# Performance work log

Measured on AMD Instinct MI355X. Metric: run time of the kernel, lower is better.

The kernel has to match this reference:

```python
import jax, jax.numpy as jnp
import numpy as np

B, S, N, D, M = 4, 4096, 16, 64, 4  # batch, seq, heads, head_dim, num_scales

def setup_inputs() -> dict:
    key = jax.random.key(0)
    ks = jax.random.split(key, 6)
    return {
        "q": jax.random.normal(ks[0], (B, S, N, D), dtype=jnp.float32),
        "k": jax.random.normal(ks[1], (B, S, N, D), dtype=jnp.float32),
        "v": jax.random.normal(ks[2], (B, S, N, D), dtype=jnp.float32),
        "memory": jax.random.normal(ks[3], (B, M, N, D, D), dtype=jnp.float32),
        "decay_factors": jax.random.uniform(ks[4], (M,), dtype=jnp.float32) + 0.5,
        "gate_weights": jax.random.uniform(ks[5], (M,), dtype=jnp.float32),
    }

def reference(q, k, v, memory, decay_factors, gate_weights):
    # --- update_memory: decayed outer-product accumulation ---
    # new_info[b,n,k,v] = sum_s k[b,s,n,k] * v[b,s,n,v]  (fused; never build [b,s,n,k,v])
    new_info = jnp.einsum('bsnk,bsnv->bnkv', k, v)
    sig = jax.nn.sigmoid(decay_factors)            # [M]
    sig5 = sig[None, :, None, None, None]          # [1,M,1,1,1]
    mem_new = memory * sig5 + (1.0 - sig5) * new_info[:, None]  # [B,M,N,D,D]
    # --- forward read: q @ memory per scale, softmax-gated scale mixing ---
    gates = jax.nn.softmax(gate_weights)           # [M]
    # fuse gate mixing into the contraction; never build [b,m,s,n,v]
    out = jnp.einsum('bsnk,bmnkv,m->bsnv', q, mem_new, gates)
    return out
```

## Files before the change

### kernel.cpp

```cpp
#include <hip/hip_runtime.h>
#include <hip/hip_bf16.h>
#include <math.h>

constexpr int B = 4, S = 4096, N = 16, D = 64, M = 4;
constexpr int SND = S * N * D;
constexpr int ND  = N * D;
constexpr int DD  = D * D;

typedef __attribute__((ext_vector_type(8))) short bf16x8;
typedef __attribute__((ext_vector_type(4))) float f32x4;
typedef unsigned short ushort_t;
typedef unsigned int uint_t;

__device__ inline ushort_t f2bf(float x) {
  __hip_bfloat16 h = __float2bfloat16(x);
  return __builtin_bit_cast(ushort_t, h);
}

__global__ __launch_bounds__(256) void k1_partials(const float* __restrict__ kg,
                                                   const float* __restrict__ vg,
                                                   float* __restrict__ part,
                                                   int spb) {
  __shared__ ushort_t kT[2][64][64];
  __shared__ ushort_t vT[2][64][64];

  const int t = threadIdx.x, w = t >> 6, l = t & 63;
  const int bn = blockIdx.x;
  const int b = bn >> 4, n = bn & 15;
  const size_t base = (size_t)b * SND + (size_t)n * D +
                      (size_t)blockIdx.y * spb * ND;

  const int ss2 = 16 * w + 2 * (l >> 3);
  const int d8  = (l & 7) * 8;
  const int m0  = (w >> 1) * 32, n0w = (w & 1) * 32;
  const int lr  = l & 15, lg = l >> 4;

  f32x4 acc[2][2];
#pragma unroll
  for (int i = 0; i < 2; ++i)
#pragma unroll
    for (int j = 0; j < 2; ++j) acc[i][j] = (f32x4)0.f;

  float ka[8], kb2[8], va[8], vb2[8];

#define K1_LOAD(st)                                                         \
  {                                                                         \
    const float* kp = kg + base + (size_t)((st) * 64 + ss2) * ND + d8;      \
    const float* vp = vg + base + (size_t)((st) * 64 + ss2) * ND + d8;      \
    *(float4*)&ka[0]  = *(const float4*)kp;                                 \
    *(float4*)&ka[4]  = *(const float4*)(kp + 4);                           \
    *(float4*)&kb2[0] = *(const float4*)(kp + ND);                          \
    *(float4*)&kb2[4] = *(const float4*)(kp + ND + 4);                      \
    *(float4*)&va[0]  = *(const float4*)vp;                                 \
    *(float4*)&va[4]  = *(const float4*)(vp + 4);                           \
    *(float4*)&vb2[0] = *(const float4*)(vp + ND);                          \
    *(float4*)&vb2[4] = *(const float4*)(vp + ND + 4);                      \
  }

#define K1_WRITE(buf)                                                       \
  {                                                                         \
    const int sl = ss2 >> 3, sw = ss2 & 7;                                  \
    _Pragma("unroll")                                                       \
    for (int i = 0; i < 8; ++i) {                                           \
      const int off = (((sl) ^ i) << 3) + sw;               \
      *(uint_t*)&kT[buf][d8 + i][off] =                                     \
          (uint_t)f2bf(ka[i]) | ((uint_t)f2bf(kb2[i]) << 16);               \
      *(uint_t*)&vT[buf][d8 + i][off] =                                     \
          (uint_t)f2bf(va[i]) | ((uint_t)f2bf(vb2[i]) << 16);               \
    }                                                                       \
  }

  K1_LOAD(0);
  K1_WRITE(0);

  const int nst = spb >> 6;
  for (int st = 0; st < nst; ++st) {
    if (st + 1 < nst) K1_LOAD(st + 1);
    __syncthreads();
    const int buf = st & 1;
#pragma unroll
    for (int ks = 0; ks < 2; ++ks) {
      const int sp = ((4 * ks + lg) ^ (lr & 7)) << 3;
      bf16x8 a0 = *(const bf16x8*)&kT[buf][m0 + lr][sp];
      bf16x8 a1 = *(const bf16x8*)&kT[buf][m0 + 16 + lr][sp];
      bf16x8 b0 = *(const bf16x8*)&vT[buf][n0w + lr][sp];
      bf16x8 b1 = *(const bf16x8*)&vT[buf][n0w + 16 + lr][sp];
      acc[0][0] = __builtin_amdgcn_mfma_f32_16x16x32_bf16(a0, b0, acc[0][0], 0, 0, 0);
      acc[0][1] = __builtin_amdgcn_mfma_f32_16x16x32_bf16(a0, b1, acc[0][1], 0, 0, 0);
      acc[1][0] = __builtin_amdgcn_mfma_f32_16x16x32_bf16(a1, b0, acc[1][0], 0, 0, 0);
      acc[1][1] = __builtin_amdgcn_mfma_f32_16x16x32_bf16(a1, b1, acc[1][1], 0, 0, 0);
    }
    if (st + 1 < nst) K1_WRITE((st + 1) & 1);
  }

  float* p = part + ((size_t)bn * gridDim.y + blockIdx.y) * DD;
#pragma unroll
  for (int mi = 0; mi < 2; ++mi)
#pragma unroll
    for (int ni = 0; ni < 2; ++ni)
#pragma unroll
      for (int ri = 0; ri < 4; ++ri)
        p[(m0 + 16 * mi + 4 * lg + ri) * 64 + (n0w + 16 * ni + lr)] =
            acc[mi][ni][ri];
#undef K1_LOAD
#undef K1_WRITE
}

__global__ __launch_bounds__(256) void k2_combine(const float* __restrict__ part,
                                                  const float* __restrict__ memg,
                                                  const float* __restrict__ decay,
                                                  const float* __restrict__ gatew,
                                                  ushort_t* __restrict__ meffT,
                                                  int nchunks) {
  const int t = threadIdx.x;
  const int bn = blockIdx.x;
  const int b = bn >> 4, n = bn & 15;
  const int kv = blockIdx.y * 256 + t;
  const int k = kv >> 6, v = kv & 63;

  float gw[M], df[M];
#pragma unroll
  for (int m = 0; m < M; ++m) { gw[m] = gatew[m]; df[m] = decay[m]; }
  const float mx = fmaxf(fmaxf(gw[0], gw[1]), fmaxf(gw[2], gw[3]));
  float e[M], esum = 0.f;
#pragma unroll
  for (int m = 0; m < M; ++m) { e[m] = expf(gw[m] - mx); esum += e[m]; }
  float wgt[M], c = 0.f;
#pragma unroll
  for (int m = 0; m < M; ++m) {
    const float g = e[m] / esum;
    const float sg = 1.f / (1.f + expf(-df[m]));
    wgt[m] = g * sg;
    c += g * (1.f - sg);
  }

  const float* pb = part + (size_t)bn * nchunks * DD + kv;
  float ni = 0.f;
  for (int ch = 0; ch < nchunks; ++ch) ni += pb[(size_t)ch * DD];
  float a = c * ni;
#pragma unroll
  for (int m = 0; m < M; ++m)
    a += wgt[m] * memg[(((size_t)b * M + m) * N + n) * DD + kv];

  meffT[(size_t)bn * DD + v * 64 + k] = f2bf(a);
}

__global__ __launch_bounds__(256, 4) void k3_out(const float* __restrict__ qg,
                                                 const ushort_t* __restrict__ meffT,
                                                 float* __restrict__ outg) {
  const int t = threadIdx.x, w = t >> 6, l = t & 63;
  const int lr = l & 15, lg = l >> 4;
  const int bn = blockIdx.x;
  const int b = bn >> 4, n = bn & 15;
  const int s0 = blockIdx.y * 256 + w * 64;

  const ushort_t* mb = meffT + (size_t)bn * DD;
  bf16x8 bfr[4][2];
#pragma unroll
  for (int ni = 0; ni < 4; ++ni)
#pragma unroll
    for (int ks = 0; ks < 2; ++ks)
      bfr[ni][ks] = *(const bf16x8*)(mb + (16 * ni + lr) * 64 + 32 * ks + 8 * lg);

  f32x4 acc[4][4];
#pragma unroll
  for (int i = 0; i < 4; ++i)
#pragma unroll
    for (int j = 0; j < 4; ++j) acc[i][j] = (f32x4)0.f;

  const size_t qbase = (size_t)b * SND + (size_t)n * D;

#pragma unroll
  for (int mi = 0; mi < 4; ++mi) {
    const float* qr = qg + qbase + (size_t)(s0 + 16 * mi + lr) * ND + 8 * lg;
#pragma unroll
    for (int ks = 0; ks < 2; ++ks) {
      float qa[8];
      *(float4*)&qa[0] = *(const float4*)(qr + 32 * ks);
      *(float4*)&qa[4] = *(const float4*)(qr + 32 * ks + 4);
      bf16x8 a;
#pragma unroll
      for (int j = 0; j < 8; ++j) a[j] = (short)f2bf(qa[j]);
#pragma unroll
      for (int ni = 0; ni < 4; ++ni)
        acc[mi][ni] = __builtin_amdgcn_mfma_f32_16x16x32_bf16(a, bfr[ni][ks],
                                                              acc[mi][ni], 0, 0, 0);
    }
  }

#pragma unroll
  for (int mi = 0; mi < 4; ++mi)
#pragma unroll
    for (int ni = 0; ni < 4; ++ni)
#pragma unroll
      for (int ri = 0; ri < 4; ++ri)
        outg[qbase + (size_t)(s0 + 16 * mi + 4 * lg + ri) * ND + 16 * ni + lr] =
            acc[mi][ni][ri];
}

extern "C" void kernel_launch(void* const* d_in, const int* in_sizes, int n_in,
                              void* d_out, int out_size, void* d_ws, size_t ws_size,
                              hipStream_t stream) {
  const float* q     = (const float*)d_in[0];
  const float* k     = (const float*)d_in[1];
  const float* v     = (const float*)d_in[2];
  const float* memg  = (const float*)d_in[3];
  const float* decay = (const float*)d_in[4];
  const float* gatew = (const float*)d_in[5];
  float* out = (float*)d_out;

  ushort_t* meffT = (ushort_t*)d_ws;
  const size_t meffT_bytes = (size_t)64 * DD * sizeof(ushort_t);
  float* part = (float*)((char*)d_ws + meffT_bytes);

  const size_t avail = ws_size > meffT_bytes ? ws_size - meffT_bytes : 0;
  int nchunks = 16;
  while (nchunks > 1 && (size_t)nchunks * 64 * DD * sizeof(float) > avail)
    nchunks >>= 1;
  const int spb = S / nchunks;

  hipLaunchKernelGGL(k1_partials, dim3(64, nchunks), dim3(256), 0, stream,
                     k, v, part, spb);
  hipLaunchKernelGGL(k2_combine, dim3(64, 16), dim3(256), 0, stream,
                     part, memg, decay, gatew, meffT, nchunks);
  hipLaunchKernelGGL(k3_out, dim3(64, 16), dim3(256), 0, stream,
                     q, meffT, out);
}
```

Before: 71.27 us.

## Give each wave its own sequence slice in k1 and reduce partials in LDS

The k/v outer-product kernel now gives each of the four waves a private 128-row sequence slice and a full 64x64 accumulator tile. Each wave double-buffers its own LDS region, so the per-stage block-wide __syncthreads is gone, and the four wave partials are summed through LDS before a single store. The chunk count is fixed at 8 instead of 16, which halves the k1 grid and the partial traffic read by k2. In exchange k1 launches fewer blocks, so parallelism drops, each thread holds more accumulator registers, and the workspace-size fallback is removed.

```diff
diff --git a/kernel.cpp b/kernel.cpp
--- a/kernel.cpp
+++ b/kernel.cpp
@@ -6,112 +6,132 @@
 constexpr int SND = S * N * D;
 constexpr int ND  = N * D;
 constexpr int DD  = D * D;
+constexpr int NCH = 8;
+constexpr int SPB = S / NCH;
 
 typedef __attribute__((ext_vector_type(8))) short bf16x8;
 typedef __attribute__((ext_vector_type(4))) float f32x4;
-typedef unsigned short ushort_t;
-typedef unsigned int uint_t;
-
-__device__ inline ushort_t f2bf(float x) {
+typedef unsigned short u16;
+typedef unsigned int u32;
+
+__device__ inline u16 f2bf(float x) {
   __hip_bfloat16 h = __float2bfloat16(x);
-  return __builtin_bit_cast(ushort_t, h);
+  return __builtin_bit_cast(u16, h);
 }
 
 __global__ __launch_bounds__(256) void k1_partials(const float* __restrict__ kg,
                                                    const float* __restrict__ vg,
-                                                   float* __restrict__ part,
-                                                   int spb) {
-  __shared__ ushort_t kT[2][64][64];
-  __shared__ ushort_t vT[2][64][64];
+                                                   float* __restrict__ part) {
+  __shared__ u16 lds[4][2][2][64][32];
 
   const int t = threadIdx.x, w = t >> 6, l = t & 63;
   const int bn = blockIdx.x;
   const int b = bn >> 4, n = bn & 15;
+  const int r = l & 7, c = l >> 3;
+  const int lr = l & 15, lg = l >> 4;
+
   const size_t base = (size_t)b * SND + (size_t)n * D +
-                      (size_t)blockIdx.y * spb * ND;
-
-  const int ss2 = 16 * w + 2 * (l >> 3);
-  const int d8  = (l & 7) * 8;
-  const int m0  = (w >> 1) * 32, n0w = (w & 1) * 32;
-  const int lr  = l & 15, lg = l >> 4;
-
-  f32x4 acc[2][2];
-#pragma unroll
-  for (int i = 0; i < 2; ++i)
-#pragma unroll
-    for (int j = 0; j < 2; ++j) acc[i][j] = (f32x4)0.f;
-
-  float ka[8], kb2[8], va[8], vb2[8];
-
-#define K1_LOAD(st)                                                         \
-  {                                                                         \
-    const float* kp = kg + base + (size_t)((st) * 64 + ss2) * ND + d8;      \
-    const float* vp = vg + base + (size_t)((st) * 64 + ss2) * ND + d8;      \
-    *(float4*)&ka[0]  = *(const float4*)kp;                                 \
-    *(float4*)&ka[4]  = *(const float4*)(kp + 4);                           \
-    *(float4*)&kb2[0] = *(const float4*)(kp + ND);                          \
-    *(float4*)&kb2[4] = *(const float4*)(kp + ND + 4);                      \
-    *(float4*)&va[0]  = *(const float4*)vp;                                 \
-    *(float4*)&va[4]  = *(const float4*)(vp + 4);                           \
-    *(float4*)&vb2[0] = *(const float4*)(vp + ND);                          \
-    *(float4*)&vb2[4] = *(const float4*)(vp + ND + 4);                      \
-  }
-
-#define K1_WRITE(buf)                                                       \
-  {                                                                         \
-    const int sl = ss2 >> 3, sw = ss2 & 7;                                  \
-    _Pragma("unroll")                                                       \
-    for (int i = 0; i < 8; ++i) {                                           \
-      const int off = (((sl) ^ i) << 3) + sw;               \
-      *(uint_t*)&kT[buf][d8 + i][off] =                                     \
-          (uint_t)f2bf(ka[i]) | ((uint_t)f2bf(kb2[i]) << 16);               \
-      *(uint_t*)&vT[buf][d8 + i][off] =                                     \
-          (uint_t)f2bf(va[i]) | ((uint_t)f2bf(vb2[i]) << 16);               \
-    }                                                                       \
-  }
-
-  K1_LOAD(0);
-  K1_WRITE(0);
-
-  const int nst = spb >> 6;
-  for (int st = 0; st < nst; ++st) {
-    if (st + 1 < nst) K1_LOAD(st + 1);
-    __syncthreads();
-    const int buf = st & 1;
-#pragma unroll
-    for (int ks = 0; ks < 2; ++ks) {
-      const int sp = ((4 * ks + lg) ^ (lr & 7)) << 3;
-      bf16x8 a0 = *(const bf16x8*)&kT[buf][m0 + lr][sp];
-      bf16x8 a1 = *(const bf16x8*)&kT[buf][m0 + 16 + lr][sp];
-      bf16x8 b0 = *(const bf16x8*)&vT[buf][n0w + lr][sp];
-      bf16x8 b1 = *(const bf16x8*)&vT[buf][n0w + 16 + lr][sp];
-      acc[0][0] = __builtin_amdgcn_mfma_f32_16x16x32_bf16(a0, b0, acc[0][0], 0, 0, 0);
-      acc[0][1] = __builtin_amdgcn_mfma_f32_16x16x32_bf16(a0, b1, acc[0][1], 0, 0, 0);
-      acc[1][0] = __builtin_amdgcn_mfma_f32_16x16x32_bf16(a1, b0, acc[1][0], 0, 0, 0);
-      acc[1][1] = __builtin_amdgcn_mfma_f32_16x16x32_bf16(a1, b1, acc[1][1], 0, 0, 0);
-    }
-    if (st + 1 < nst) K1_WRITE((st + 1) & 1);
-  }
-
-  float* p = part + ((size_t)bn * gridDim.y + blockIdx.y) * DD;
-#pragma unroll
-  for (int mi = 0; mi < 2; ++mi)
-#pragma unroll
-    for (int ni = 0; ni < 2; ++ni)
+                      ((size_t)blockIdx.y * SPB + (size_t)w * 128) * ND;
+
+  f32x4 acc[4][4];
+#pragma unroll
+  for (int i = 0; i < 4; ++i)
+#pragma unroll
+    for (int j = 0; j < 4; ++j) acc[i][j] = (f32x4)0.f;
+
+  float kfa[2][2][8], vfa[2][2][8];
+
+#define STAGE_LOAD(tt)                                                        \
+  {                                                                           \
+    _Pragma("unroll") for (int h = 0; h < 2; ++h)                             \
+    _Pragma("unroll") for (int sp = 0; sp < 2; ++sp) {                        \
+      const float* kp =                                                       \
+          kg + base + (size_t)((tt) * 32 + 16 * h + 2 * r + sp) * ND + 8 * c; \
+      const float* vp =                                                       \
+          vg + base + (size_t)((tt) * 32 + 16 * h + 2 * r + sp) * ND + 8 * c; \
+      *(float4*)&kfa[h][sp][0] = *(const float4*)kp;                          \
+      *(float4*)&kfa[h][sp][4] = *(const float4*)(kp + 4);                    \
+      *(float4*)&vfa[h][sp][0] = *(const float4*)vp;                          \
+      *(float4*)&vfa[h][sp][4] = *(const float4*)(vp + 4);                    \
+    }                                                                         \
+  }
+
+#define STAGE_WRITE(buf)                                                      \
+  {                                                                           \
+    _Pragma("unroll") for (int h = 0; h < 2; ++h)                             \
+    _Pragma("unroll") for (int dd = 0; dd < 8; ++dd) {                        \
+      const int d = 8 * c + dd;                                               \
+      const int slot = (((2 * h + (r >> 2)) ^ (d & 3)) << 3) + ((2 * r) & 7); \
+      *(u32*)&lds[w][buf][0][d][slot] =                                       \
+          (u32)f2bf(kfa[h][0][dd]) | ((u32)f2bf(kfa[h][1][dd]) << 16);        \
+      *(u32*)&lds[w][buf][1][d][slot] =                                       \
+          (u32)f2bf(vfa[h][0][dd]) | ((u32)f2bf(vfa[h][1][dd]) << 16);        \
+    }                                                                         \
+  }
+
+#define COMPUTE(buf)                                                          \
+  {                                                                           \
+    bf16x8 af[4], bfq[4];                                                     \
+    _Pragma("unroll") for (int mi = 0; mi < 4; ++mi) {                        \
+      const int row = 16 * mi + lr;                                           \
+      af[mi]  = *(const bf16x8*)&lds[w][buf][0][row][(lg ^ (row & 3)) << 3];  \
+      bfq[mi] = *(const bf16x8*)&lds[w][buf][1][row][(lg ^ (row & 3)) << 3];  \
+    }                                                                         \
+    _Pragma("unroll") for (int mi = 0; mi < 4; ++mi)                          \
+    _Pragma("unroll") for (int ni = 0; ni < 4; ++ni)                          \
+      acc[mi][ni] = __builtin_amdgcn_mfma_f32_16x16x32_bf16(                  \
+          af[mi], bfq[ni], acc[mi][ni], 0, 0, 0);                             \
+  }
+
+  STAGE_LOAD(0);
+  STAGE_WRITE(0);
+  STAGE_LOAD(1);
+  COMPUTE(0);
+  STAGE_WRITE(1);
+  STAGE_LOAD(2);
+  COMPUTE(1);
+  STAGE_WRITE(0);
+  STAGE_LOAD(3);
+  COMPUTE(0);
+  STAGE_WRITE(1);
+  COMPUTE(1);
+
+#undef STAGE_LOAD
+#undef STAGE_WRITE
+#undef COMPUTE
+
+  __syncthreads();
+  float* red = (float*)lds;
+#pragma unroll
+  for (int mi = 0; mi < 4; ++mi)
+#pragma unroll
+    for (int ni = 0; ni < 4; ++ni)
 #pragma unroll
       for (int ri = 0; ri < 4; ++ri)
-        p[(m0 + 16 * mi + 4 * lg + ri) * 64 + (n0w + 16 * ni + lr)] =
+        red[w * 4096 + (16 * mi + 4 * lg + ri) * 64 + 16 * ni + lr] =
             acc[mi][ni][ri];
-#undef K1_LOAD
-#undef K1_WRITE
+  __syncthreads();
+
+  float* p = part + ((size_t)bn * NCH + blockIdx.y) * DD;
+#pragma unroll
+  for (int j = 0; j < 4; ++j) {
+    const int e = t * 16 + 4 * j;
+    const float4 a0 = *(const float4*)&red[e];
+    const float4 a1 = *(const float4*)&red[4096 + e];
+    const float4 a2 = *(const float4*)&red[8192 + e];
+    const float4 a3 = *(const float4*)&red[12288 + e];
+    *(float4*)&p[e] = make_float4(a0.x + a1.x + a2.x + a3.x,
+                                  a0.y + a1.y + a2.y + a3.y,
+                                  a0.z + a1.z + a2.z + a3.z,
+                                  a0.w + a1.w + a2.w + a3.w);
+  }
 }
 
 __global__ __launch_bounds__(256) void k2_combine(const float* __restrict__ part,
                                                   const float* __restrict__ memg,
                                                   const float* __restrict__ decay,
                                                   const float* __restrict__ gatew,
-                                                  ushort_t* __restrict__ meffT,
-                                                  int nchunks) {
+                                                  u16* __restrict__ meffT) {
   const int t = threadIdx.x;
   const int bn = blockIdx.x;
   const int b = bn >> 4, n = bn & 15;
@@ -125,19 +145,20 @@
   float e[M], esum = 0.f;
 #pragma unroll
   for (int m = 0; m < M; ++m) { e[m] = expf(gw[m] - mx); esum += e[m]; }
-  float wgt[M], c = 0.f;
+  float wgt[M], cc = 0.f;
 #pragma unroll
   for (int m = 0; m < M; ++m) {
     const float g = e[m] / esum;
     const float sg = 1.f / (1.f + expf(-df[m]));
     wgt[m] = g * sg;
-    c += g * (1.f - sg);
-  }
-
-  const float* pb = part + (size_t)bn * nchunks * DD + kv;
+    cc += g * (1.f - sg);
+  }
+
+  const float* pb = part + (size_t)bn * NCH * DD + kv;
   float ni = 0.f;
-  for (int ch = 0; ch < nchunks; ++ch) ni += pb[(size_t)ch * DD];
-  float a = c * ni;
+#pragma unroll
+  for (int ch = 0; ch < NCH; ++ch) ni += pb[(size_t)ch * DD];
+  float a = cc * ni;
 #pragma unroll
   for (int m = 0; m < M; ++m)
     a += wgt[m] * memg[(((size_t)b * M + m) * N + n) * DD + kv];
@@ -146,7 +167,7 @@
 }
 
 __global__ __launch_bounds__(256, 4) void k3_out(const float* __restrict__ qg,
-                                                 const ushort_t* __restrict__ meffT,
+                                                 const u16* __restrict__ meffT,
                                                  float* __restrict__ outg) {
   const int t = threadIdx.x, w = t >> 6, l = t & 63;
   const int lr = l & 15, lg = l >> 4;
@@ -154,7 +175,7 @@
   const int b = bn >> 4, n = bn & 15;
   const int s0 = blockIdx.y * 256 + w * 64;
 
-  const ushort_t* mb = meffT + (size_t)bn * DD;
+  const u16* mb = meffT + (size_t)bn * DD;
   bf16x8 bfr[4][2];
 #pragma unroll
   for (int ni = 0; ni < 4; ++ni)
@@ -209,20 +230,14 @@
   const float* gatew = (const float*)d_in[5];
   float* out = (float*)d_out;
 
-  ushort_t* meffT = (ushort_t*)d_ws;
-  const size_t meffT_bytes = (size_t)64 * DD * sizeof(ushort_t);
+  u16* meffT = (u16*)d_ws;
+  const size_t meffT_bytes = (size_t)64 * DD * sizeof(u16);
   float* part = (float*)((char*)d_ws + meffT_bytes);
 
-  const size_t avail = ws_size > meffT_bytes ? ws_size - meffT_bytes : 0;
-  int nchunks = 16;
-  while (nchunks > 1 && (size_t)nchunks * 64 * DD * sizeof(float) > avail)
-    nchunks >>= 1;
-  const int spb = S / nchunks;
-
-  hipLaunchKernelGGL(k1_partials, dim3(64, nchunks), dim3(256), 0, stream,
-                     k, v, part, spb);
+  hipLaunchKernelGGL(k1_partials, dim3(64, NCH), dim3(256), 0, stream,
+                     k, v, part);
   hipLaunchKernelGGL(k2_combine, dim3(64, 16), dim3(256), 0, stream,
-                     part, memg, decay, gatew, meffT, nchunks);
+                     part, memg, decay, gatew, meffT);
   hipLaunchKernelGGL(k3_out, dim3(64, 16), dim3(256), 0, stream,
                      q, meffT, out);
 }
```

Result: faster. 64.83 us (-9.0%).
